# Performance work log

Measured on AMD Instinct MI355X. Metric: run time of the kernel, lower is better.

## Reference

```python
import jax, jax.numpy as jnp
import numpy as np

N = 100000      # nodes
E = 3200000     # edges
IN_DIM = 128
HID = 128
OUT_DIM = 1
LAYERS = 8
ALPHA = 0.1
THETA = 0.5


def setup_inputs() -> dict:
    key = jax.random.key(0)
    ks = jax.random.split(key, 8)
    x = jax.random.normal(ks[0], (N, IN_DIM), dtype=jnp.float32)
    edge_index = jax.random.randint(ks[1], (2, E), 0, N, dtype=jnp.int64)
    edge_weight = jax.random.uniform(ks[2], (E,), dtype=jnp.float32)  # unused by original forward path
    W_in = jax.random.normal(ks[3], (IN_DIM, HID), dtype=jnp.float32) * 0.05
    b_in = jnp.zeros((HID,), dtype=jnp.float32)
    W_gcn = jax.random.normal(ks[4], (LAYERS, HID, HID), dtype=jnp.float32) * 0.05
    W_out = jax.random.normal(ks[5], (HID, OUT_DIM), dtype=jnp.float32) * 0.05
    b_out = jnp.zeros((OUT_DIM,), dtype=jnp.float32)
    return {"x": x, "edge_weight": edge_weight, "W_in": W_in, "b_in": b_in,
            "W_gcn": W_gcn, "W_out": W_out, "b_out": b_out, "edge_index": edge_index}


def _gcn_norm(edge_index, dtype):
    # add self loops (fill value 1), symmetric normalization deg^-1/2 A deg^-1/2
    sl = jnp.arange(N, dtype=edge_index.dtype)
    row = jnp.concatenate([edge_index[0], sl])
    col = jnp.concatenate([edge_index[1], sl])
    w = jnp.ones(row.shape[0], dtype=dtype)
    deg = jax.ops.segment_sum(w, col, num_segments=N)
    dinv = jnp.where(deg > 0, jax.lax.rsqrt(deg), 0.0)
    norm = dinv[row] * dinv[col]
    return row, col, norm


def reference(x, edge_weight, W_in, b_in, W_gcn, W_out, b_out, edge_index):
    row, col, norm = _gcn_norm(edge_index, x.dtype)
    h = x @ W_in + b_in            # initial_proj
    h0 = h                          # residual x0
    for i in range(LAYERS):
        # dropout is identity in eval mode
        msg = h[row] * norm[:, None]                       # gather + scale [E+N, HID]
        agg = jax.ops.segment_sum(msg, col, num_segments=N)
        s = (1.0 - ALPHA) * agg + ALPHA * h0               # identity-mapped residual
        beta = float(np.log(THETA / (i + 1) + 1.0))
        h = (1.0 - beta) * s + beta * (s @ W_gcn[i])       # GCNII weight mix
        h = jax.nn.relu(h)
    return h @ W_out + b_out
```

## Files before the change

kernel.cpp:

```cpp
#include <hip/hip_runtime.h>
#include <hip/hip_bf16.h>
#include <math.h>

#define N_NODES 100000
#define N_EDGES 3200000
#define HID 128
#define LAYERS 8
#define ALPHA 0.1f
#define THETA 0.5f

#define NBKT 391
#define BKT_STRIDE 10240
#define EPT 16
#define CHUNK 4096

typedef unsigned int uint;
typedef unsigned short ushort;
typedef __attribute__((ext_vector_type(8))) short short8;
typedef __attribute__((ext_vector_type(4))) float f32x4;

__device__ inline float bf_lo(uint p) { return __uint_as_float(p << 16); }
__device__ inline float bf_hi(uint p) { return __uint_as_float(p & 0xffff0000u); }
__device__ inline uint bf_pack(float x, float y) {
    uint ux = __float_as_uint(x), uy = __float_as_uint(y);
    uint rx = (ux + 0x7fffu + ((ux >> 16) & 1u)) >> 16;
    uint ry = (uy + 0x7fffu + ((uy >> 16) & 1u)) >> 16;
    return rx | (ry << 16);
}
__device__ inline ushort bfr(float x) {
    uint u = __float_as_uint(x);
    return (ushort)((u + 0x7fffu + ((u >> 16) & 1u)) >> 16);
}
__device__ inline float bff(ushort s) { return __uint_as_float(((uint)s) << 16); }

__global__ __launch_bounds__(256) void k_bucket(const int* __restrict__ rowi,
                                                const int* __restrict__ coli,
                                                uint* __restrict__ eb,
                                                int* __restrict__ gcnt) {
    __shared__ int bcnt[NBKT];
    __shared__ int gbase[NBKT];
    int t = threadIdx.x;
    for (int i = t; i < NBKT; i += 256) bcnt[i] = 0;
    __syncthreads();

    int e0 = blockIdx.x * CHUNK;
    int bk[EPT];
    int rk[EPT];
    uint rec[EPT];
#pragma unroll
    for (int j = 0; j < EPT; ++j) {
        int e = e0 + j * 256 + t;
        if (e < N_EDGES) {
            int r = rowi[e];
            int c = coli[e];
            bk[j] = c >> 8;
            rec[j] = ((uint)r << 8) | (uint)(c & 255);
            rk[j] = atomicAdd(&bcnt[bk[j]], 1);
        } else {
            bk[j] = -1;
        }
    }
    __syncthreads();
    for (int i = t; i < NBKT; i += 256) {
        int n = bcnt[i];
        gbase[i] = n ? atomicAdd(&gcnt[i], n) : 0;
    }
    __syncthreads();
#pragma unroll
    for (int j = 0; j < EPT; ++j) {
        if (bk[j] >= 0)
            eb[(size_t)bk[j] * BKT_STRIDE + gbase[bk[j]] + rk[j]] = rec[j];
    }
}

__global__ __launch_bounds__(512) void k_bscan(const int* __restrict__ gcnt,
                                               int* __restrict__ bbase) {
    __shared__ int lds[512];
    int t = threadIdx.x;
    int v = (t < NBKT) ? gcnt[t] : 0;
    lds[t] = v;
    __syncthreads();
    for (int off = 1; off < 512; off <<= 1) {
        int u = (t >= off) ? lds[t - off] : 0;
        __syncthreads();
        lds[t] += u;
        __syncthreads();
    }
    if (t < NBKT) bbase[t] = lds[t] - v;
}

__global__ __launch_bounds__(256) void k_node_ipt(const uint* __restrict__ eb,
                                                  const int* __restrict__ gcnt,
                                                  const int* __restrict__ bbase,
                                                  float* __restrict__ dinv,
                                                  int* __restrict__ indptr) {
    __shared__ int ncnt[256];
    __shared__ int sc[256];
    int b = blockIdx.x;
    int t = threadIdx.x;
    ncnt[t] = 0;
    __syncthreads();
    int ne = gcnt[b];
    const uint* ebp = eb + (size_t)b * BKT_STRIDE;
    for (int i = t; i < ne; i += 256) atomicAdd(&ncnt[ebp[i] & 255], 1);
    __syncthreads();
    int v = ncnt[t];
    sc[t] = v;
    __syncthreads();
    for (int off = 1; off < 256; off <<= 1) {
        int u = (t >= off) ? sc[t - off] : 0;
        __syncthreads();
        sc[t] += u;
        __syncthreads();
    }
    int node = b * 256 + t;
    if (node < N_NODES) {
        dinv[node] = rsqrtf((float)(v + 1));
        indptr[node] = bbase[b] + (sc[t] - v);
    }
    if (b == NBKT - 1 && t == 255) indptr[N_NODES] = N_EDGES;
}

__global__ __launch_bounds__(256) void k_fill2(const uint* __restrict__ eb,
                                               const int* __restrict__ gcnt,
                                               const float* __restrict__ dinv,
                                               const int* __restrict__ indptr,
                                               int2* __restrict__ csr) {
    __shared__ float sdv[256];
    __shared__ int scur[256];
    __shared__ int sipt[256];
    int b = blockIdx.x;
    int t = threadIdx.x;
    int node = b * 256 + t;
    sdv[t] = (node < N_NODES) ? dinv[node] : 0.f;
    sipt[t] = (node < N_NODES) ? indptr[node] : 0;
    scur[t] = 0;
    __syncthreads();
    int ne = gcnt[b];
    const uint* ebp = eb + (size_t)b * BKT_STRIDE;
    for (int i = t; i < ne; i += 256) {
        uint rec = ebp[i];
        int lc = rec & 255;
        int r = (int)(rec >> 8);
        int pos = sipt[lc] + atomicAdd(&scur[lc], 1);
        csr[pos] = make_int2(r, __float_as_int(dinv[r] * sdv[lc]));
    }
}

__global__ __launch_bounds__(256) void k_wprep(const float* __restrict__ Wg,
                                               ushort* __restrict__ Wt) {
    int l = blockIdx.x;
    const float* W = Wg + (size_t)l * HID * HID;
    ushort* T = Wt + (size_t)l * HID * HID;
    int t = threadIdx.x;
#pragma unroll
    for (int i = 0; i < 16; ++i) {
        int idx = t + 256 * i;
        int k = idx >> 5;
        int c4 = idx & 31;
        float4 v = *(const float4*)(W + (size_t)k * HID + c4 * 4);
        T[(c4 * 4 + 0) * HID + k] = bfr(v.x);
        T[(c4 * 4 + 1) * HID + k] = bfr(v.y);
        T[(c4 * 4 + 2) * HID + k] = bfr(v.z);
        T[(c4 * 4 + 3) * HID + k] = bfr(v.w);
    }
}

__global__ __launch_bounds__(256) void k_spmm(const uint* __restrict__ h,
                                              const uint* __restrict__ h0,
                                              const float* __restrict__ dinv,
                                              const int* __restrict__ indptr,
                                              const int2* __restrict__ csr,
                                              uint* __restrict__ s_out) {
    int node = blockIdx.x * 8 + (threadIdx.x >> 5);
    if (node >= N_NODES) return;
    int l = threadIdx.x & 31;
    int beg = indptr[node];
    int end = indptr[node + 1];
    float di = dinv[node];
    uint2 hs = *(const uint2*)(h + node * 64 + l * 2);
    uint2 h0v = *(const uint2*)(h0 + node * 64 + l * 2);
    float a0[2] = {0.f, 0.f}, a1[2] = {0.f, 0.f};
    float a2[2] = {0.f, 0.f}, a3[2] = {0.f, 0.f};
    int e = beg;
    for (; e + 8 <= end; e += 8) {
        int2 rr[8];
#pragma unroll
        for (int j = 0; j < 8; ++j) rr[j] = csr[e + j];
        uint2 p[8];
#pragma unroll
        for (int j = 0; j < 8; ++j) p[j] = *(const uint2*)(h + rr[j].x * 64 + l * 2);
#pragma unroll
        for (int j = 0; j < 8; ++j) {
            float w = __int_as_float(rr[j].y);
            int d = j & 1;
            a0[d] = fmaf(w, bf_lo(p[j].x), a0[d]);
            a1[d] = fmaf(w, bf_hi(p[j].x), a1[d]);
            a2[d] = fmaf(w, bf_lo(p[j].y), a2[d]);
            a3[d] = fmaf(w, bf_hi(p[j].y), a3[d]);
        }
    }
    for (; e < end; e += 2) {
        int2 rr[2];
        float w[2];
#pragma unroll
        for (int j = 0; j < 2; ++j) {
            int idx = e + j;
            rr[j] = csr[idx < end ? idx : beg];
            w[j] = (idx < end) ? __int_as_float(rr[j].y) : 0.f;
        }
        uint2 p[2];
#pragma unroll
        for (int j = 0; j < 2; ++j) p[j] = *(const uint2*)(h + rr[j].x * 64 + l * 2);
#pragma unroll
        for (int j = 0; j < 2; ++j) {
            a0[j] = fmaf(w[j], bf_lo(p[j].x), a0[j]);
            a1[j] = fmaf(w[j], bf_hi(p[j].x), a1[j]);
            a2[j] = fmaf(w[j], bf_lo(p[j].y), a2[j]);
            a3[j] = fmaf(w[j], bf_hi(p[j].y), a3[j]);
        }
    }
    float s0 = a0[0] + a0[1];
    float s1 = a1[0] + a1[1];
    float s2 = a2[0] + a2[1];
    float s3 = a3[0] + a3[1];
    float selfw = di * di;
    float rx = (1.0f - ALPHA) * fmaf(selfw, bf_lo(hs.x), s0) + ALPHA * bf_lo(h0v.x);
    float ry = (1.0f - ALPHA) * fmaf(selfw, bf_hi(hs.x), s1) + ALPHA * bf_hi(h0v.x);
    float rz = (1.0f - ALPHA) * fmaf(selfw, bf_lo(hs.y), s2) + ALPHA * bf_lo(h0v.y);
    float rw = (1.0f - ALPHA) * fmaf(selfw, bf_hi(hs.y), s3) + ALPHA * bf_hi(h0v.y);
    uint2 o;
    o.x = bf_pack(rx, ry);
    o.y = bf_pack(rz, rw);
    *(uint2*)(s_out + node * 64 + l * 2) = o;
}

__global__ __launch_bounds__(256) void k_gemm_in(const float* __restrict__ A,
                                                 const float* __restrict__ W,
                                                 const float* __restrict__ bias,
                                                 uint* __restrict__ out0,
                                                 uint* __restrict__ out1) {
    __shared__ float sT[32 * 64];
    __shared__ float Ws[32 * 128];
    int t = threadIdx.x;
    int tr = t & 15;
    int tc = t >> 4;
    int rowBase = blockIdx.x * 64;
    float acc[4][8] = {};

    for (int ko = 0; ko < HID; ko += 32) {
#pragma unroll
        for (int pass = 0; pass < 2; ++pass) {
            int lin = t + 256 * pass;
            int r = lin >> 3;
            int kq = lin & 7;
            int ar = rowBase + r;
            if (ar >= N_NODES) ar = N_NODES - 1;
            float4 v = *(const float4*)(A + (size_t)ar * HID + ko + 4 * kq);
            sT[(4 * kq + 0) * 64 + r] = v.x;
            sT[(4 * kq + 1) * 64 + r] = v.y;
            sT[(4 * kq + 2) * 64 + r] = v.z;
            sT[(4 * kq + 3) * 64 + r] = v.w;
        }
#pragma unroll
        for (int pass = 0; pass < 4; ++pass) {
            int lin = t + 256 * pass;
            int k = lin >> 5;
            int c4 = lin & 31;
            *(float4*)&Ws[k * 128 + 4 * c4] =
                *(const float4*)(W + (size_t)(ko + k) * HID + 4 * c4);
        }
        __syncthreads();
#pragma unroll
        for (int k = 0; k < 32; ++k) {
            float4 a = *(const float4*)&sT[k * 64 + 4 * tr];
            float4 w0 = *(const float4*)&Ws[k * 128 + 8 * tc];
            float4 w1 = *(const float4*)&Ws[k * 128 + 8 * tc + 4];
            float av[4] = {a.x, a.y, a.z, a.w};
            float wv[8] = {w0.x, w0.y, w0.z, w0.w, w1.x, w1.y, w1.z, w1.w};
#pragma unroll
            for (int i = 0; i < 4; ++i)
#pragma unroll
                for (int j = 0; j < 8; ++j)
                    acc[i][j] = fmaf(av[i], wv[j], acc[i][j]);
        }
        __syncthreads();
    }

    int c0 = 8 * tc;
    float bb[8];
#pragma unroll
    for (int j = 0; j < 8; ++j) bb[j] = bias[c0 + j];
#pragma unroll
    for (int i = 0; i < 4; ++i) {
        int r = rowBase + 4 * tr + i;
        if (r >= N_NODES) break;
        float v[8];
#pragma unroll
        for (int j = 0; j < 8; ++j) v[j] = acc[i][j] + bb[j];
        uint4 o;
        o.x = bf_pack(v[0], v[1]);
        o.y = bf_pack(v[2], v[3]);
        o.z = bf_pack(v[4], v[5]);
        o.w = bf_pack(v[6], v[7]);
        *(uint4*)(out0 + (size_t)r * 64 + c0 / 2) = o;
        *(uint4*)(out1 + (size_t)r * 64 + c0 / 2) = o;
    }
}

#define SAS 136

__global__ __launch_bounds__(256) void k_gemm_layer(const uint* __restrict__ A,
                                                    const ushort* __restrict__ Wt,
                                                    uint* __restrict__ out0,
                                                    float beta) {
    __shared__ ushort sA[64 * SAS];
    __shared__ ushort pack[64 * 128];
    int t = threadIdx.x;
    int lane = t & 63;
    int wv = t >> 6;
    int rowBase = blockIdx.x * 64;

#pragma unroll
    for (int i = 0; i < 4; ++i) {
        int idx = t + 256 * i;
        int r = idx >> 4;
        int q = idx & 15;
        int ar = rowBase + r;
        if (ar >= N_NODES) ar = N_NODES - 1;
        uint4 v = *(const uint4*)(A + (size_t)ar * 64 + q * 4);
        *(uint4*)((uint*)(sA + r * SAS) + q * 4) = v;
    }
    __syncthreads();

    int fr = lane & 15;
    int fq = lane >> 4;
    const ushort* Wb0 = Wt + (size_t)(wv * 32 + fr) * HID;
    const ushort* Wb1 = Wt + (size_t)(wv * 32 + 16 + fr) * HID;
    f32x4 acc[4][2] = {};
#pragma unroll
    for (int kc = 0; kc < 4; ++kc) {
        int kof = kc * 32 + fq * 8;
        short8 b0 = *(const short8*)(Wb0 + kof);
        short8 b1 = *(const short8*)(Wb1 + kof);
#pragma unroll
        for (int tm = 0; tm < 4; ++tm) {
            short8 a = *(const short8*)(sA + (tm * 16 + fr) * SAS + kof);
            acc[tm][0] = __builtin_amdgcn_mfma_f32_16x16x32_bf16(a, b0, acc[tm][0], 0, 0, 0);
            acc[tm][1] = __builtin_amdgcn_mfma_f32_16x16x32_bf16(a, b1, acc[tm][1], 0, 0, 0);
        }
    }

    float ob = 1.0f - beta;
#pragma unroll
    for (int tm = 0; tm < 4; ++tm)
#pragma unroll
        for (int tn = 0; tn < 2; ++tn)
#pragma unroll
            for (int r = 0; r < 4; ++r) {
                int row = tm * 16 + fq * 4 + r;
                int col = wv * 32 + tn * 16 + fr;
                float sv = bff(sA[row * SAS + col]);
                float val = fmaxf(fmaf(ob, sv, beta * acc[tm][tn][r]), 0.f);
                pack[row * 128 + col] = bfr(val);
            }
    __syncthreads();
#pragma unroll
    for (int i = 0; i < 4; ++i) {
        int idx = t + 256 * i;
        int r = idx >> 4;
        int q = idx & 15;
        int ar = rowBase + r;
        if (ar < N_NODES)
            *(uint4*)(out0 + (size_t)ar * 64 + q * 4) =
                *(const uint4*)((const uint*)(pack + r * 128) + q * 4);
    }
}

__global__ __launch_bounds__(256) void k_out(const uint* __restrict__ h,
                                             const float* __restrict__ W_out,
                                             const float* __restrict__ b_out,
                                             float* __restrict__ out) {
    int node = blockIdx.x * 4 + (threadIdx.x >> 6);
    if (node >= N_NODES) return;
    int lane = threadIdx.x & 63;
    uint p = h[node * 64 + lane];
    float2 wv = *(const float2*)(W_out + lane * 2);
    float pr = bf_lo(p) * wv.x + bf_hi(p) * wv.y;
#pragma unroll
    for (int off = 32; off > 0; off >>= 1) pr += __shfl_down(pr, off);
    if (lane == 0) out[node] = pr + b_out[0];
}

extern "C" void kernel_launch(void* const* d_in, const int* in_sizes, int n_in,
                              void* d_out, int out_size, void* d_ws, size_t ws_size,
                              hipStream_t stream) {
    const float* x     = (const float*)d_in[0];
    const float* W_in  = (const float*)d_in[2];
    const float* b_in  = (const float*)d_in[3];
    const float* W_gcn = (const float*)d_in[4];
    const float* W_out = (const float*)d_in[5];
    const float* b_out = (const float*)d_in[6];
    const int*   ei    = (const int*)d_in[7];
    const int* rowi = ei;
    const int* coli = ei + N_EDGES;
    float* out = (float*)d_out;

    char* ws = (char*)d_ws;
    auto alloc = [&](size_t bytes) -> char* {
        char* p = ws;
        ws += (bytes + 255) & ~(size_t)255;
        return p;
    };
    float*  dinv    = (float*) alloc((size_t)N_NODES * 4);
    int*    indptr  = (int*)   alloc((size_t)(N_NODES + 1) * 4);
    int*    gcnt    = (int*)   alloc(2048 * 4);
    int*    bbase   = (int*)   alloc(2048 * 4);
    int2*   csr     = (int2*)  alloc((size_t)N_EDGES * 8);
    ushort* Wt      = (ushort*)alloc((size_t)LAYERS * HID * HID * 2);
    uint*   hA      = (uint*)  alloc((size_t)N_NODES * 64 * 4);
    uint*   hB      = (uint*)  alloc((size_t)N_NODES * 64 * 4);
    uint*   h0      = (uint*)  alloc((size_t)N_NODES * 64 * 4);
    uint*   eb      = hB;

    hipMemsetAsync(gcnt, 0, (size_t)NBKT * 4, stream);

    k_bucket<<<(N_EDGES + CHUNK - 1) / CHUNK, 256, 0, stream>>>(rowi, coli, eb, gcnt);
    k_bscan<<<1, 512, 0, stream>>>(gcnt, bbase);
    k_node_ipt<<<NBKT, 256, 0, stream>>>(eb, gcnt, bbase, dinv, indptr);
    k_fill2<<<NBKT, 256, 0, stream>>>(eb, gcnt, dinv, indptr, csr);
    k_wprep<<<LAYERS, 256, 0, stream>>>(W_gcn, Wt);

    int gemm_blocks = (N_NODES + 63) / 64;
    k_gemm_in<<<gemm_blocks, 256, 0, stream>>>(x, W_in, b_in, h0, hA);

    uint* hin = hA;
    uint* hout = hB;
    for (int l = 0; l < LAYERS; ++l) {
        k_spmm<<<(N_NODES + 7) / 8, 256, 0, stream>>>(hin, h0, dinv, indptr,
                                                      csr, hout);
        float beta = logf(THETA / (float)(l + 1) + 1.0f);
        k_gemm_layer<<<gemm_blocks, 256, 0, stream>>>(
            hout, Wt + (size_t)l * HID * HID, hin, beta);
    }
    k_out<<<(N_NODES + 3) / 4, 256, 0, stream>>>(hin, W_out, b_out, out);
}
```

Baseline: 1.352 ms.

## Store column indices only in CSR, fuse output projection into last GEMM

Edge weights are no longer stored in the CSR array. The SpMM gathers dinv[src] per edge and applies the destination dinv once at the end, which halves CSR index traffic per layer at the cost of an extra small gather. The separate output-projection kernel is folded into the final layer GEMM, so the last hidden state is never written and re-read. The duplicate write of the initial projection is removed by reading h0 directly in layer 0.

```diff
diff --git a/kernel.cpp b/kernel.cpp
--- a/kernel.cpp
+++ b/kernel.cpp
@@ -123,16 +123,13 @@
 
 __global__ __launch_bounds__(256) void k_fill2(const uint* __restrict__ eb,
                                                const int* __restrict__ gcnt,
-                                               const float* __restrict__ dinv,
                                                const int* __restrict__ indptr,
-                                               int2* __restrict__ csr) {
-    __shared__ float sdv[256];
+                                               int* __restrict__ csr) {
     __shared__ int scur[256];
     __shared__ int sipt[256];
     int b = blockIdx.x;
     int t = threadIdx.x;
     int node = b * 256 + t;
-    sdv[t] = (node < N_NODES) ? dinv[node] : 0.f;
     sipt[t] = (node < N_NODES) ? indptr[node] : 0;
     scur[t] = 0;
     __syncthreads();
@@ -141,9 +138,8 @@
     for (int i = t; i < ne; i += 256) {
         uint rec = ebp[i];
         int lc = rec & 255;
-        int r = (int)(rec >> 8);
         int pos = sipt[lc] + atomicAdd(&scur[lc], 1);
-        csr[pos] = make_int2(r, __float_as_int(dinv[r] * sdv[lc]));
+        csr[pos] = (int)(rec >> 8);
     }
 }
 
@@ -170,7 +166,7 @@
                                               const uint* __restrict__ h0,
                                               const float* __restrict__ dinv,
                                               const int* __restrict__ indptr,
-                                              const int2* __restrict__ csr,
+                                              const int* __restrict__ csr,
                                               uint* __restrict__ s_out) {
     int node = blockIdx.x * 8 + (threadIdx.x >> 5);
     if (node >= N_NODES) return;
@@ -184,15 +180,18 @@
     float a2[2] = {0.f, 0.f}, a3[2] = {0.f, 0.f};
     int e = beg;
     for (; e + 8 <= end; e += 8) {
-        int2 rr[8];
-#pragma unroll
-        for (int j = 0; j < 8; ++j) rr[j] = csr[e + j];
+        int sr[8];
+#pragma unroll
+        for (int j = 0; j < 8; ++j) sr[j] = csr[e + j];
+        float dv[8];
+#pragma unroll
+        for (int j = 0; j < 8; ++j) dv[j] = dinv[sr[j]];
         uint2 p[8];
 #pragma unroll
-        for (int j = 0; j < 8; ++j) p[j] = *(const uint2*)(h + rr[j].x * 64 + l * 2);
+        for (int j = 0; j < 8; ++j) p[j] = *(const uint2*)(h + sr[j] * 64 + l * 2);
 #pragma unroll
         for (int j = 0; j < 8; ++j) {
-            float w = __int_as_float(rr[j].y);
+            float w = dv[j];
             int d = j & 1;
             a0[d] = fmaf(w, bf_lo(p[j].x), a0[d]);
             a1[d] = fmaf(w, bf_hi(p[j].x), a1[d]);
@@ -201,17 +200,17 @@
         }
     }
     for (; e < end; e += 2) {
-        int2 rr[2];
+        int sr[2];
         float w[2];
 #pragma unroll
         for (int j = 0; j < 2; ++j) {
             int idx = e + j;
-            rr[j] = csr[idx < end ? idx : beg];
-            w[j] = (idx < end) ? __int_as_float(rr[j].y) : 0.f;
+            sr[j] = csr[idx < end ? idx : beg];
+            w[j] = (idx < end) ? dinv[sr[j]] : 0.f;
         }
         uint2 p[2];
 #pragma unroll
-        for (int j = 0; j < 2; ++j) p[j] = *(const uint2*)(h + rr[j].x * 64 + l * 2);
+        for (int j = 0; j < 2; ++j) p[j] = *(const uint2*)(h + sr[j] * 64 + l * 2);
 #pragma unroll
         for (int j = 0; j < 2; ++j) {
             a0[j] = fmaf(w[j], bf_lo(p[j].x), a0[j]);
@@ -224,11 +223,11 @@
     float s1 = a1[0] + a1[1];
     float s2 = a2[0] + a2[1];
     float s3 = a3[0] + a3[1];
-    float selfw = di * di;
-    float rx = (1.0f - ALPHA) * fmaf(selfw, bf_lo(hs.x), s0) + ALPHA * bf_lo(h0v.x);
-    float ry = (1.0f - ALPHA) * fmaf(selfw, bf_hi(hs.x), s1) + ALPHA * bf_hi(h0v.x);
-    float rz = (1.0f - ALPHA) * fmaf(selfw, bf_lo(hs.y), s2) + ALPHA * bf_lo(h0v.y);
-    float rw = (1.0f - ALPHA) * fmaf(selfw, bf_hi(hs.y), s3) + ALPHA * bf_hi(h0v.y);
+    float sc = (1.0f - ALPHA) * di;
+    float rx = sc * fmaf(di, bf_lo(hs.x), s0) + ALPHA * bf_lo(h0v.x);
+    float ry = sc * fmaf(di, bf_hi(hs.x), s1) + ALPHA * bf_hi(h0v.x);
+    float rz = sc * fmaf(di, bf_lo(hs.y), s2) + ALPHA * bf_lo(h0v.y);
+    float rw = sc * fmaf(di, bf_hi(hs.y), s3) + ALPHA * bf_hi(h0v.y);
     uint2 o;
     o.x = bf_pack(rx, ry);
     o.y = bf_pack(rz, rw);
@@ -238,8 +237,7 @@
 __global__ __launch_bounds__(256) void k_gemm_in(const float* __restrict__ A,
                                                  const float* __restrict__ W,
                                                  const float* __restrict__ bias,
-                                                 uint* __restrict__ out0,
-                                                 uint* __restrict__ out1) {
+                                                 uint* __restrict__ out0) {
     __shared__ float sT[32 * 64];
     __shared__ float Ws[32 * 128];
     int t = threadIdx.x;
@@ -304,7 +302,6 @@
         o.z = bf_pack(v[4], v[5]);
         o.w = bf_pack(v[6], v[7]);
         *(uint4*)(out0 + (size_t)r * 64 + c0 / 2) = o;
-        *(uint4*)(out1 + (size_t)r * 64 + c0 / 2) = o;
     }
 }
 
@@ -313,9 +310,13 @@
 __global__ __launch_bounds__(256) void k_gemm_layer(const uint* __restrict__ A,
                                                     const ushort* __restrict__ Wt,
                                                     uint* __restrict__ out0,
-                                                    float beta) {
+                                                    float beta,
+                                                    const float* __restrict__ Wo,
+                                                    const float* __restrict__ b_out,
+                                                    float* __restrict__ outf) {
     __shared__ ushort sA[64 * SAS];
     __shared__ ushort pack[64 * 128];
+    __shared__ float sWo[128];
     int t = threadIdx.x;
     int lane = t & 63;
     int wv = t >> 6;
@@ -331,6 +332,7 @@
         uint4 v = *(const uint4*)(A + (size_t)ar * 64 + q * 4);
         *(uint4*)((uint*)(sA + r * SAS) + q * 4) = v;
     }
+    if (Wo != nullptr && t < 128) sWo[t] = Wo[t];
     __syncthreads();
 
     int fr = lane & 15;
@@ -365,31 +367,34 @@
                 pack[row * 128 + col] = bfr(val);
             }
     __syncthreads();
-#pragma unroll
-    for (int i = 0; i < 4; ++i) {
-        int idx = t + 256 * i;
-        int r = idx >> 4;
-        int q = idx & 15;
-        int ar = rowBase + r;
-        if (ar < N_NODES)
-            *(uint4*)(out0 + (size_t)ar * 64 + q * 4) =
-                *(const uint4*)((const uint*)(pack + r * 128) + q * 4);
-    }
-}
-
-__global__ __launch_bounds__(256) void k_out(const uint* __restrict__ h,
-                                             const float* __restrict__ W_out,
-                                             const float* __restrict__ b_out,
-                                             float* __restrict__ out) {
-    int node = blockIdx.x * 4 + (threadIdx.x >> 6);
-    if (node >= N_NODES) return;
-    int lane = threadIdx.x & 63;
-    uint p = h[node * 64 + lane];
-    float2 wv = *(const float2*)(W_out + lane * 2);
-    float pr = bf_lo(p) * wv.x + bf_hi(p) * wv.y;
-#pragma unroll
-    for (int off = 32; off > 0; off >>= 1) pr += __shfl_down(pr, off);
-    if (lane == 0) out[node] = pr + b_out[0];
+
+    if (Wo == nullptr) {
+#pragma unroll
+        for (int i = 0; i < 4; ++i) {
+            int idx = t + 256 * i;
+            int r = idx >> 4;
+            int q = idx & 15;
+            int ar = rowBase + r;
+            if (ar < N_NODES)
+                *(uint4*)(out0 + (size_t)ar * 64 + q * 4) =
+                    *(const uint4*)((const uint*)(pack + r * 128) + q * 4);
+        }
+    } else {
+        int row = t >> 2;
+        int sub = t & 3;
+        const ushort* pr_row = pack + row * 128 + sub * 32;
+        float pr = 0.f;
+#pragma unroll
+        for (int i = 0; i < 32; i += 2) {
+            uint pp = *(const uint*)(pr_row + i);
+            pr = fmaf(bf_lo(pp), sWo[sub * 32 + i], pr);
+            pr = fmaf(bf_hi(pp), sWo[sub * 32 + i + 1], pr);
+        }
+        pr += __shfl_xor(pr, 1);
+        pr += __shfl_xor(pr, 2);
+        int ar = rowBase + row;
+        if (sub == 0 && ar < N_NODES) outf[ar] = pr + b_out[0];
+    }
 }
 
 extern "C" void kernel_launch(void* const* d_in, const int* in_sizes, int n_in,
@@ -416,7 +421,7 @@
     int*    indptr  = (int*)   alloc((size_t)(N_NODES + 1) * 4);
     int*    gcnt    = (int*)   alloc(2048 * 4);
     int*    bbase   = (int*)   alloc(2048 * 4);
-    int2*   csr     = (int2*)  alloc((size_t)N_EDGES * 8);
+    int*    csr     = (int*)   alloc((size_t)N_EDGES * 4);
     ushort* Wt      = (ushort*)alloc((size_t)LAYERS * HID * HID * 2);
     uint*   hA      = (uint*)  alloc((size_t)N_NODES * 64 * 4);
     uint*   hB      = (uint*)  alloc((size_t)N_NODES * 64 * 4);
@@ -428,20 +433,20 @@
     k_bucket<<<(N_EDGES + CHUNK - 1) / CHUNK, 256, 0, stream>>>(rowi, coli, eb, gcnt);
     k_bscan<<<1, 512, 0, stream>>>(gcnt, bbase);
     k_node_ipt<<<NBKT, 256, 0, stream>>>(eb, gcnt, bbase, dinv, indptr);
-    k_fill2<<<NBKT, 256, 0, stream>>>(eb, gcnt, dinv, indptr, csr);
+    k_fill2<<<NBKT, 256, 0, stream>>>(eb, gcnt, indptr, csr);
     k_wprep<<<LAYERS, 256, 0, stream>>>(W_gcn, Wt);
 
     int gemm_blocks = (N_NODES + 63) / 64;
-    k_gemm_in<<<gemm_blocks, 256, 0, stream>>>(x, W_in, b_in, h0, hA);
-
-    uint* hin = hA;
-    uint* hout = hB;
+    k_gemm_in<<<gemm_blocks, 256, 0, stream>>>(x, W_in, b_in, h0);
+
     for (int l = 0; l < LAYERS; ++l) {
-        k_spmm<<<(N_NODES + 7) / 8, 256, 0, stream>>>(hin, h0, dinv, indptr,
-                                                      csr, hout);
+        const uint* hsrc = (l == 0) ? h0 : hA;
+        k_spmm<<<(N_NODES + 7) / 8, 256, 0, stream>>>(hsrc, h0, dinv, indptr,
+                                                      csr, hB);
         float beta = logf(THETA / (float)(l + 1) + 1.0f);
+        bool last = (l == LAYERS - 1);
         k_gemm_layer<<<gemm_blocks, 256, 0, stream>>>(
-            hout, Wt + (size_t)l * HID * HID, hin, beta);
-    }
-    k_out<<<(N_NODES + 3) / 4, 256, 0, stream>>>(hin, W_out, b_out, out);
-}
+            hB, Wt + (size_t)l * HID * HID, hA, beta,
+            last ? W_out : nullptr, b_out, out);
+    }
+}
```

Result: faster. 1.298 ms (-4.0%).
